# Performance work log

Hardware: AMD Instinct MI355X
Metric: run time of the kernel (lower is better)

## Reference

```python
import jax, jax.numpy as jnp
import numpy as np

B, T, S, H, V, MAXL = 8, 128, 256, 1024, 32000, 512
STD = 0.02


def _ln(x, g, b):
    m = jnp.mean(x, -1, keepdims=True)
    v = jnp.mean((x - m) ** 2, -1, keepdims=True)
    return (x - m) / jnp.sqrt(v + 1e-5) * g + b


def setup_inputs() -> dict:
    key = jax.random.key(0)
    ks = jax.random.split(key, 16)
    n = lambda k, shape: jax.random.normal(k, shape, jnp.float32) * STD
    inp = {
        "input_ids": jax.random.randint(ks[0], (B, T), 0, V),
        "encoder_hidden_states": jax.random.normal(ks[1], (B, S, H), jnp.float32),
        "pattern_masks": jax.random.randint(ks[2], (B, T, V), 0, 2).astype(bool),
        "attention_mask": jnp.ones((B, S), bool),
        "tok_emb": n(ks[3], (V, H)),
        "pos_emb": n(ks[4], (MAXL, H)),
        "w_ih": n(ks[5], (4 * H, H)),
        "w_hh": n(ks[6], (4 * H, H)),
        "b_ih": jnp.zeros((4 * H,), jnp.float32),
        "b_hh": jnp.zeros((4 * H,), jnp.float32),
        "wq": n(ks[7], (H, H)), "bq": jnp.zeros((H,), jnp.float32),
        "wk": n(ks[8], (H, H)), "bk": jnp.zeros((H,), jnp.float32),
        "wc": n(ks[9], (H, 2 * H)), "bc": jnp.zeros((H,), jnp.float32),
        "wo": n(ks[10], (V, H)), "bo": jnp.zeros((V,), jnp.float32),
        "g1": n(ks[11], (H,)), "be1": jnp.zeros((H,), jnp.float32),
        "g2": n(ks[12], (H,)), "be2": jnp.zeros((H,), jnp.float32),
    }
    return inp


def reference(input_ids, encoder_hidden_states, pattern_masks, attention_mask,
              tok_emb, pos_emb, w_ih, w_hh, b_ih, b_hh,
              wq, bq, wk, bk, wc, bc, wo, bo, g1, be1, g2, be2):
    # Token + positional embedding (dropout is identity in eval)
    x = tok_emb[input_ids] + pos_emb[:T][None, :, :]  # [B,T,H]

    # Single-layer LSTM (PyTorch gate order i,f,g,o) via scan over time
    def step(carry, xt):
        h, c = carry
        gates = xt @ w_ih.T + b_ih + h @ w_hh.T + b_hh
        i, f, g, o = jnp.split(gates, 4, axis=-1)
        c = jax.nn.sigmoid(f) * c + jax.nn.sigmoid(i) * jnp.tanh(g)
        h = jax.nn.sigmoid(o) * jnp.tanh(c)
        return (h, c), h

    h0 = jnp.zeros((B, H), x.dtype)
    _, hs = jax.lax.scan(step, (h0, h0), jnp.swapaxes(x, 0, 1))
    lstm_out = jnp.swapaxes(hs, 0, 1)  # [B,T,H]

    # Attention: per-position loop in torch == batched over T (keys invariant)
    qn = _ln(lstm_out @ wq.T + bq, g1, be1)              # [B,T,H]
    kn = _ln(encoder_hidden_states @ wk.T + bk, g1, be1)  # [B,S,H]
    scale = H ** (-0.5) * 0.5
    scores = jnp.einsum('bth,bsh->bts', qn, kn) * scale
    am = attention_mask[:, None, :]
    scores = jnp.where(am, scores, -10000.0)
    mx = jnp.max(scores, -1, keepdims=True)
    ex = jnp.exp(scores - mx)
    ex = jnp.where(am, ex, 0.0)
    w = ex / (jnp.sum(ex, -1, keepdims=True) + 1e-6)
    ctx = jnp.einsum('bts,bsh->bth', w, kn)              # [B,T,H]

    hidden = _ln(jnp.concatenate([lstm_out, ctx], -1) @ wc.T + bc, g2, be2)
    logits = hidden @ wo.T + bo                           # [B,T,V]
    logits = jnp.where(pattern_masks, logits, -10000.0)
    return logits
```

## Files before the change

### kernel.cpp

```cpp
#include <hip/hip_runtime.h>
#include <cstdint>
#include <cstddef>

#define Bdim 8
#define Tdim 128
#define Sdim 256
#define Hdim 1024
#define Vdim 32000
#define SENT 0xFFFFFFFFFFFFFFFFULL

typedef unsigned short u16;
typedef unsigned long long u64;
typedef __attribute__((ext_vector_type(8))) short short8;
typedef __attribute__((ext_vector_type(4))) short short4v;
typedef __attribute__((ext_vector_type(4))) float f32x4;
typedef __attribute__((ext_vector_type(2))) unsigned long long u64x2;

union Frag { short8 v; short4v h[2]; };

__device__ __forceinline__ float bf2f(u16 u){
  union { unsigned int i; float f; } x; x.i = ((unsigned int)u) << 16; return x.f;
}
__device__ __forceinline__ u16 f2b(float f){
  union { float f; unsigned int u; } x; x.f = f;
  unsigned int r = x.u + 0x7FFFu + ((x.u >> 16) & 1u);
  return (u16)(r >> 16);
}
__device__ __forceinline__ float ftanh(float x){
  x = fminf(10.f, fmaxf(-10.f, x));
  const float e = __expf(2.f * x);
  return (e - 1.f) / (e + 1.f);
}

__device__ __forceinline__ void gload16(const void* g, void* l){
  __builtin_amdgcn_global_load_lds((const __attribute__((address_space(1))) unsigned int*)g,
                                   (__attribute__((address_space(3))) unsigned int*)l, 16, 0, 0);
}

__device__ __forceinline__ int qsw(int r){ return (r + (r >> 2)) & 3; }

__device__ __forceinline__ u64 aload(const u64* p){
  return __hip_atomic_load(p, __ATOMIC_RELAXED, __HIP_MEMORY_SCOPE_AGENT);
}
__device__ __forceinline__ void astore(u64* p, u64 v){
  __hip_atomic_store(p, v, __ATOMIC_RELAXED, __HIP_MEMORY_SCOPE_AGENT);
}

__device__ __forceinline__ bool mask_at(const void* m, size_t idx, int byteflag){
  if (byteflag) return ((const unsigned char*)m)[idx] != 0;
  return ((const int*)m)[idx] != 0;
}

template<typename OutT, bool BF32, int MASK, int NT>
__device__ __forceinline__ void gemm_core(
    char* ldsA0, char* ldsB0, char* ldsA1, char* ldsB1,
    int m0, int n0, int z,
    const u16* __restrict__ A, int lda, long sA,
    const void* __restrict__ Bp, int ldb, long sB,
    OutT* __restrict__ C, int ldc, long sC,
    const float* __restrict__ bias,
    const void* __restrict__ mask,
    const int* __restrict__ mflag,
    int K, float alpha)
{
  const int tid  = threadIdx.x;
  const int lane = tid & 63, wid = tid >> 6;
  const int lm = lane & 15, lg = lane >> 4;
  const int wm = wid >> 1, wn = wid & 1;
  const char* Ab = (const char*)(A + (size_t)z * sA);

  f32x4 acc[4][4 * NT];
#pragma unroll
  for (int i = 0; i < 4; i++)
#pragma unroll
    for (int j = 0; j < 4 * NT; j++) acc[i][j] = (f32x4){0.f, 0.f, 0.f, 0.f};

  const int brow = tid >> 1, bhalf = tid & 1;
  const int qb_st = qsw(brow);

  auto stageA = [&](char* dst, int k0){
    const char* ga = Ab + ((size_t)m0 * lda + k0) * 2;
    const int f0 = tid, f1 = tid + 256;
    const int r0 = f0 >> 2, r1 = f1 >> 2;
    gload16(ga + (size_t)r0 * (lda * 2) + ((f0 & 3) ^ qsw(r0)) * 16, dst + (f0 & ~63) * 16);
    gload16(ga + (size_t)r1 * (lda * 2) + ((f1 & 3) ^ qsw(r1)) * 16, dst + (f1 & ~63) * 16);
  };
  auto stageB16 = [&](char* dst, int k0){
    const char* gbase = (const char*)((const u16*)Bp + (size_t)z * sB);
#pragma unroll
    for (int s = 0; s < NT; s++) {
      const char* gb = gbase + ((size_t)(n0 + s * 128) * ldb + k0) * 2;
      const int f0 = tid, f1 = tid + 256;
      const int r0 = f0 >> 2, r1 = f1 >> 2;
      gload16(gb + (size_t)r0 * (ldb * 2) + ((f0 & 3) ^ qsw(r0)) * 16, dst + s * 8192 + (f0 & ~63) * 16);
      gload16(gb + (size_t)r1 * (ldb * 2) + ((f1 & 3) ^ qsw(r1)) * 16, dst + s * 8192 + (f1 & ~63) * 16);
    }
  };

  float4 nv0, nv1, nv2, nv3;
  auto loadB32 = [&](int k0){
    const float* Bf = (const float*)Bp + (size_t)z * sB;
    const float4* src = (const float4*)(Bf + (size_t)(n0 + brow) * ldb + k0 + bhalf * 16);
    nv0 = src[0]; nv1 = src[1]; nv2 = src[2]; nv3 = src[3];
  };
  auto writeB32 = [&](char* dst){
    union { short8 v; short s[8]; } p0, p1;
    p0.s[0]=(short)f2b(nv0.x); p0.s[1]=(short)f2b(nv0.y); p0.s[2]=(short)f2b(nv0.z); p0.s[3]=(short)f2b(nv0.w);
    p0.s[4]=(short)f2b(nv1.x); p0.s[5]=(short)f2b(nv1.y); p0.s[6]=(short)f2b(nv1.z); p0.s[7]=(short)f2b(nv1.w);
    p1.s[0]=(short)f2b(nv2.x); p1.s[1]=(short)f2b(nv2.y); p1.s[2]=(short)f2b(nv2.z); p1.s[3]=(short)f2b(nv2.w);
    p1.s[4]=(short)f2b(nv3.x); p1.s[5]=(short)f2b(nv3.y); p1.s[6]=(short)f2b(nv3.z); p1.s[7]=(short)f2b(nv3.w);
    char* base = dst + brow * 64;
    *(short8*)(base + (((bhalf * 2 + 0) ^ qb_st) * 16)) = p0.v;
    *(short8*)(base + (((bhalf * 2 + 1) ^ qb_st) * 16)) = p1.v;
  };

  stageA(ldsA0, 0);
  if (BF32) { loadB32(0); writeB32(ldsB0); }
  else stageB16(ldsB0, 0);
  __syncthreads();

  char *cA = ldsA0, *cB = ldsB0, *nA = ldsA1, *nB = ldsB1;
  const int nk = K >> 5;
  for (int i = 0; i < nk; i++) {
    const bool more = (i + 1) < nk;
    if (more) {
      stageA(nA, (i + 1) << 5);
      if (BF32) loadB32((i + 1) << 5);
      else stageB16(nB, (i + 1) << 5);
    }
    Frag a[4];
#pragma unroll
    for (int mi = 0; mi < 4; mi++) {
      const int rr = wm * 64 + mi * 16 + lm;
      const int q = qsw(rr);
      const char* p = cA + rr * 64 + (lg & 1) * 8;
      a[mi].h[0] = *(const short4v*)(p + (((lg >> 1) ^ q) * 16));
      a[mi].h[1] = *(const short4v*)(p + ((((lg >> 1) | 2) ^ q) * 16));
    }
#pragma unroll
    for (int ni = 0; ni < 4 * NT; ni++) {
      const int s = ni >> 2, nl = ni & 3;
      const int rr = wn * 64 + nl * 16 + lm;
      const int q = qsw(rr);
      const char* p = cB + s * 8192 + rr * 64 + (lg & 1) * 8;
      Frag b;
      b.h[0] = *(const short4v*)(p + (((lg >> 1) ^ q) * 16));
      b.h[1] = *(const short4v*)(p + ((((lg >> 1) | 2) ^ q) * 16));
#pragma unroll
      for (int mi = 0; mi < 4; mi++)
        acc[mi][ni] = __builtin_amdgcn_mfma_f32_16x16x32_bf16(a[mi].v, b.v, acc[mi][ni], 0, 0, 0);
    }
    if (BF32 && more) writeB32(nB);
    __syncthreads();
    char* t;
    t = cA; cA = nA; nA = t;
    t = cB; cB = nB; nB = t;
  }

  const int bflag = (MASK == 1) ? *mflag : 0;
#pragma unroll
  for (int mi = 0; mi < 4; mi++) {
#pragma unroll
    for (int ni = 0; ni < 4 * NT; ni++) {
      const int row = m0 + wm * 64 + mi * 16 + lg * 4;
      const int col = n0 + (ni >> 2) * 128 + wn * 64 + (ni & 3) * 16 + lm;
      const float bb = bias ? bias[col] : 0.f;
#pragma unroll
      for (int j = 0; j < 4; j++) {
        float v = acc[mi][ni][j] * alpha + bb;
        const size_t midx = (size_t)(row + j) * ldc + col;
        if (MASK == 1) { if (!mask_at(mask, midx, bflag)) v = -10000.0f; }
        if (MASK == 2) { if (!((const unsigned char*)mask)[midx]) v = -10000.0f; }
        const size_t o = (size_t)z * sC + midx;
        if constexpr (sizeof(OutT) == 2) C[o] = (OutT)f2b(v); else C[o] = (OutT)v;
      }
    }
  }
}

template<typename OutT, bool BF32, int MASK, bool SWAP, int NT = 1>
__global__ __launch_bounds__(256) void gemm_bt(
    const u16* __restrict__ A, int lda, long sA,
    const void* __restrict__ Bp, int ldb, long sB,
    OutT* __restrict__ C, int ldc, long sC,
    const float* __restrict__ bias,
    const void* __restrict__ mask,
    const int* __restrict__ mflag,
    int K, float alpha)
{
  __shared__ alignas(16) char lds[(8192 + 8192 * NT) * 2];
  const int m0 = (SWAP ? blockIdx.x : blockIdx.y) * 128;
  const int n0 = (SWAP ? blockIdx.y : blockIdx.x) * (128 * NT);
  char* ldsA1 = lds + 8192 + 8192 * NT;
  gemm_core<OutT, BF32, MASK, NT>(lds, lds + 8192, ldsA1, ldsA1 + 8192,
      m0, n0, blockIdx.z, A, lda, sA, Bp, ldb, sB, C, ldc, sC,
      bias, mask, mflag, K, alpha);
}

__device__ void lstm_body(char* smem,
    const u16* __restrict__ xpre, const u16* __restrict__ whh,
    u16* __restrict__ hbuf, u16* __restrict__ cat, int bx)
{
  u16* wlds = (u16*)smem;
  u16* hlds = (u16*)(smem + 131072);
  const int tid = threadIdx.x, lane = tid & 63, wid = tid >> 6;
  const int lm = lane & 15, lg = lane >> 4;
  const int gcol0 = bx * 64;

  for (int q = tid; q < 8192; q += 256) {
    const int r = q >> 7, cc = q & 127;
    gload16(whh + (size_t)(gcol0 + r) * 1024 + (size_t)(cc ^ (r & 7)) * 8,
            (char*)wlds + (q & ~63) * 16);
  }

  float c_reg = 0.f;
  const int rloc = wid * 16 + lm, swb = rloc & 7, swa = lm & 7;
  const u16* wl = wlds + rloc * 1024;
  const u16* hl = hlds + swa * 1024;
  const int pk = tid >> 2, qq = tid & 3;
  const u16* xp = xpre + (size_t)(lm * Tdim) * 4096 + gcol0 + wid * 16 + lg * 4;

  for (int t = 0; t < Tdim; t++) {
    u64 xw = 0;
    if (lm < 8) xw = *(const u64*)(xp + (size_t)t * 4096);
    if (t > 0) {
      const u64* ps = (const u64*)(hbuf + ((size_t)(t - 1) * 64 + pk) * 128) + qq * 8;
      u64 w0=SENT,w1=SENT,w2=SENT,w3=SENT,w4=SENT,w5=SENT,w6=SENT,w7=SENT;
      for (;;) {
        if (w0 == SENT) w0 = aload(ps + 0);
        if (w1 == SENT) w1 = aload(ps + 1);
        if (w2 == SENT) w2 = aload(ps + 2);
        if (w3 == SENT) w3 = aload(ps + 3);
        if (w4 == SENT) w4 = aload(ps + 4);
        if (w5 == SENT) w5 = aload(ps + 5);
        if (w6 == SENT) w6 = aload(ps + 6);
        if (w7 == SENT) w7 = aload(ps + 7);
        if (w0 != SENT && w1 != SENT && w2 != SENT && w3 != SENT &&
            w4 != SENT && w5 != SENT && w6 != SENT && w7 != SENT) break;
        __builtin_amdgcn_s_sleep(1);
      }
      {
        const int m = qq * 2;
        u64x2 a; a[0] = w0; a[1] = w1;
        u64x2 b; b[0] = w2; b[1] = w3;
        *(u64x2*)((char*)hlds + m * 2048 + (((pk * 2 + 0) ^ m) * 16)) = a;
        *(u64x2*)((char*)hlds + m * 2048 + (((pk * 2 + 1) ^ m) * 16)) = b;
      }
      {
        const int m = qq * 2 + 1;
        u64x2 a; a[0] = w4; a[1] = w5;
        u64x2 b; b[0] = w6; b[1] = w7;
        *(u64x2*)((char*)hlds + m * 2048 + (((pk * 2 + 0) ^ m) * 16)) = a;
        *(u64x2*)((char*)hlds + m * 2048 + (((pk * 2 + 1) ^ m) * 16)) = b;
      }
    }
    __syncthreads();

    f32x4 acc0, acc1, acc2, acc3;
    {
      union { u64 w; u16 s[4]; } xu; xu.w = xw;
      acc0[0] = bf2f(xu.s[0]); acc0[1] = bf2f(xu.s[1]);
      acc0[2] = bf2f(xu.s[2]); acc0[3] = bf2f(xu.s[3]);
    }
    acc1 = (f32x4){0.f,0.f,0.f,0.f};
    acc2 = (f32x4){0.f,0.f,0.f,0.f};
    acc3 = (f32x4){0.f,0.f,0.f,0.f};

    if (t > 0) {
#pragma unroll
      for (int kk = 0; kk < 32; kk++) {
        const int c0 = kk * 4 + (lg >> 1);
        const int sub = (lg & 1) * 4;
        Frag aw, bh;
        aw.h[0] = *(const short4v*)(wl + ((c0 ^ swb) << 3) + sub);
        aw.h[1] = *(const short4v*)(wl + (((c0 + 2) ^ swb) << 3) + sub);
        bh.h[0] = *(const short4v*)(hl + ((c0 ^ swa) << 3) + sub);
        bh.h[1] = *(const short4v*)(hl + (((c0 + 2) ^ swa) << 3) + sub);
        if ((kk & 3) == 0)      acc0 = __builtin_amdgcn_mfma_f32_16x16x32_bf16(aw.v, bh.v, acc0, 0, 0, 0);
        else if ((kk & 3) == 1) acc1 = __builtin_amdgcn_mfma_f32_16x16x32_bf16(aw.v, bh.v, acc1, 0, 0, 0);
        else if ((kk & 3) == 2) acc2 = __builtin_amdgcn_mfma_f32_16x16x32_bf16(aw.v, bh.v, acc2, 0, 0, 0);
        else                    acc3 = __builtin_amdgcn_mfma_f32_16x16x32_bf16(aw.v, bh.v, acc3, 0, 0, 0);
      }
    }
    const f32x4 g4 = (acc0 + acc1) + (acc2 + acc3);

    const float si = 1.f / (1.f + __expf(-g4[0]));
    const float sf = 1.f / (1.f + __expf(-g4[1]));
    const float so = 1.f / (1.f + __expf(-g4[3]));
    const float cn = sf * c_reg + si * ftanh(g4[2]);
    c_reg = cn;
    const float hn = so * ftanh(cn);
    const int hb = (int)f2b(hn);

    const int v0 = __shfl(hb, lm, 64);
    const int v1 = __shfl(hb, lm + 16, 64);
    const int v2 = __shfl(hb, lm + 32, 64);
    const int v3 = __shfl(hb, lm + 48, 64);
    if (lg == 0 && lm < 8) {
      const u64 pack = (u64)(v0 & 0xFFFF) | ((u64)(v1 & 0xFFFF) << 16)
                     | ((u64)(v2 & 0xFFFF) << 32) | ((u64)(v3 & 0xFFFF) << 48);
      astore((u64*)(hbuf + ((size_t)t * 64 + bx) * 128 + lm * 16 + wid * 4), pack);
      *(u64*)(cat + (size_t)(lm * Tdim + t) * 2048 + bx * 16 + wid * 4) = pack;
    }
    __syncthreads();
  }
}

__global__ __launch_bounds__(256) void lstm_plus(
    const u16* __restrict__ xpre, const u16* __restrict__ whh,
    u16* __restrict__ hbuf, u16* __restrict__ cat,
    const u16* __restrict__ encb, const u16* __restrict__ wkb,
    float* __restrict__ klin, const float* __restrict__ bk,
    const float* __restrict__ wo, u16* __restrict__ wob,
    const float* __restrict__ wq, u16* __restrict__ wqb,
    const float* __restrict__ wc, u16* __restrict__ wcb,
    const void* __restrict__ pmask, unsigned char* __restrict__ pmaskb,
    const int* __restrict__ bflag)
{
  __shared__ alignas(16) char smem[147456];
  const int bx = blockIdx.x;
  if (bx < 64) {
    lstm_body(smem, xpre, whh, hbuf, cat, bx);
  } else if (bx < 192) {
    const int idx = bx - 64;
    gemm_core<float, false, 0, 1>(smem, smem + 8192, smem + 16384, smem + 24576,
        (idx >> 3) * 128, (idx & 7) * 128, 0,
        encb, 1024, 0, wkb, 1024, 0, klin, 1024, 0, bk, nullptr, nullptr, 1024, 1.f);
  } else {
    const int s = bx - 192;
    const int tid = threadIdx.x;
    for (int r = s; r < 1024; r += 64) {
      const size_t i = (size_t)r * 1024 + tid * 4;
      const float4 v = *(const float4*)(wq + i);
      u16* op = wqb + i;
      op[0] = f2b(v.x); op[1] = f2b(v.y); op[2] = f2b(v.z); op[3] = f2b(v.w);
    }
    for (int r = s; r < 1024; r += 64) {
#pragma unroll
      for (int hc = 0; hc < 2; hc++) {
        const size_t i = (size_t)r * 2048 + hc * 1024 + tid * 4;
        const float4 v = *(const float4*)(wc + i);
        u16* op = wcb + i;
        op[0] = f2b(v.x); op[1] = f2b(v.y); op[2] = f2b(v.z); op[3] = f2b(v.w);
      }
    }
    if (wob) {
      for (int r = s; r < Vdim; r += 64) {
        const size_t i = (size_t)r * 1024 + tid * 4;
        const float4 v = *(const float4*)(wo + i);
        u16* op = wob + i;
        op[0] = f2b(v.x); op[1] = f2b(v.y); op[2] = f2b(v.z); op[3] = f2b(v.w);
      }
    }
    if (pmaskb) {
      const int bfl = *bflag;
      const size_t total = (size_t)Bdim * Tdim * Vdim;
      const size_t nthr = 64 * 256;
      if (bfl == 0) {
        for (size_t i = ((size_t)s * 256 + tid) * 4; i < total; i += nthr * 4) {
          const int4 v = *(const int4*)((const int*)pmask + i);
          uchar4 o;
          o.x = v.x ? 1 : 0; o.y = v.y ? 1 : 0; o.z = v.z ? 1 : 0; o.w = v.w ? 1 : 0;
          *(uchar4*)(pmaskb + i) = o;
        }
      } else {
        for (size_t i = ((size_t)s * 256 + tid) * 16; i < total; i += nthr * 16) {
          *(int4*)(pmaskb + i) = *(const int4*)((const unsigned char*)pmask + i);
        }
      }
    }
  }
}

__global__ __launch_bounds__(256) void prep_k(
    const float* __restrict__ w_hh, const float* __restrict__ w_ih,
    const float* __restrict__ wk,   const float* __restrict__ enc,
    const int* __restrict__ ids,
    const float* __restrict__ tok,  const float* __restrict__ pos,
    const float* __restrict__ b_ih, const float* __restrict__ b_hh,
    const unsigned char* __restrict__ pmask,
    u16* __restrict__ whhb, u16* __restrict__ wihb, u16* __restrict__ wkb,
    u16* __restrict__ encb, u16* __restrict__ xbf,
    float* __restrict__ biasf, u64* __restrict__ hbuf, int* __restrict__ bflag)
{
  __shared__ int sdet;
  const int b = blockIdx.x, tid = threadIdx.x;
  if (b < 8192) {
    const bool ih = b >= 4096;
    const int r = b & 4095;
    const int p = (r & 3) * Hdim + (r >> 2);
    const float4 v = *(const float4*)((ih ? w_ih : w_hh) + (size_t)p * Hdim + tid * 4);
    u16* op = (ih ? wihb : whhb) + (size_t)r * Hdim + tid * 4;
    op[0] = f2b(v.x); op[1] = f2b(v.y); op[2] = f2b(v.z); op[3] = f2b(v.w);
  } else if (b < 9216) {
    const size_t i = (size_t)(b - 8192) * 1024 + tid * 4;
    const float4 v = *(const float4*)(wk + i);
    u16* op = wkb + i;
    op[0] = f2b(v.x); op[1] = f2b(v.y); op[2] = f2b(v.z); op[3] = f2b(v.w);
  } else if (b < 11264) {
    const size_t i = (size_t)(b - 9216) * 1024 + tid * 4;
    const float4 v = *(const float4*)(enc + i);
    u16* op = encb + i;
    op[0] = f2b(v.x); op[1] = f2b(v.y); op[2] = f2b(v.z); op[3] = f2b(v.w);
  } else if (b < 12288) {
    const int row = b - 11264;
    const int t = row & (Tdim - 1);
    const int id = ids[row];
    const int h0 = tid * 4;
    const float4 a = *(const float4*)(tok + (size_t)id * Hdim + h0);
    const float4 p = *(const float4*)(pos + (size_t)t * Hdim + h0);
    u16* op = xbf + (size_t)row * Hdim + h0;
    op[0] = f2b(a.x + p.x); op[1] = f2b(a.y + p.y); op[2] = f2b(a.z + p.z); op[3] = f2b(a.w + p.w);
  } else if (b < 12292) {
    const int n0 = (b - 12288) * 1024 + tid * 4;
#pragma unroll
    for (int j = 0; j < 4; j++) {
      const int n = n0 + j;
      const int p = (n & 3) * Hdim + (n >> 2);
      biasf[n] = b_ih[p] + b_hh[p];
    }
  } else if (b < 12548) {
    const size_t i = ((size_t)(b - 12292) * 256 + tid) * 4;
    u64x2 s2; s2[0] = SENT; s2[1] = SENT;
    *(u64x2*)(hbuf + i)     = s2;
    *(u64x2*)(hbuf + i + 2) = s2;
  } else {
    if (tid == 0) sdet = 0;
    __syncthreads();
    int loc = 0;
    for (int i = tid; i < 65536; i += 256)
      if ((i & 3) && pmask[i]) loc = 1;
    if (loc) atomicOr(&sdet, 1);
    __syncthreads();
    if (tid == 0) bflag[0] = sdet;
  }
}

__global__ __launch_bounds__(256) void ln_rows(const float* __restrict__ in, u16* __restrict__ out,
                                               const float* __restrict__ g, const float* __restrict__ be){
  const int row = blockIdx.x, tid = threadIdx.x;
  const int lane = tid & 63, wid = tid >> 6;
  const float4 x = *(const float4*)(in + (size_t)row * Hdim + tid * 4);
  float s = x.x + x.y + x.z + x.w;
  float q = x.x * x.x + x.y * x.y + x.z * x.z + x.w * x.w;
  for (int o = 32; o; o >>= 1) { s += __shfl_down(s, o, 64); q += __shfl_down(q, o, 64); }
  __shared__ float sm[8];
  if (lane == 0) { sm[wid] = s; sm[4 + wid] = q; }
  __syncthreads();
  const float ts = sm[0] + sm[1] + sm[2] + sm[3];
  const float tq = sm[4] + sm[5] + sm[6] + sm[7];
  const float mean = ts * (1.f / Hdim);
  const float var  = tq * (1.f / Hdim) - mean * mean;
  const float r = rsqrtf(var + 1e-5f);
  const int h0 = tid * 4;
  const float4 gv = *(const float4*)(g + h0);
  const float4 bv = *(const float4*)(be + h0);
  u16* op = out + (size_t)row * Hdim + h0;
  op[0] = f2b((x.x - mean) * r * gv.x + bv.x);
  op[1] = f2b((x.y - mean) * r * gv.y + bv.y);
  op[2] = f2b((x.z - mean) * r * gv.z + bv.z);
  op[3] = f2b((x.w - mean) * r * gv.w + bv.w);
}
__global__ __launch_bounds__(256) void softmax_k(const float* __restrict__ sc, const void* __restrict__ am,
                                                 const int* __restrict__ mflag, u16* __restrict__ w){
  const int row = blockIdx.x, tid = threadIdx.x;
  const int lane = tid & 63, wid = tid >> 6;
  const int b = row >> 7;
  const int bflag = *mflag;
  const float v = sc[(size_t)row * Sdim + tid];
  const bool mk = mask_at(am, (size_t)b * Sdim + tid, bflag);
  const float vm = mk ? v : -10000.0f;
  float mx = vm;
  for (int o = 32; o; o >>= 1) mx = fmaxf(mx, __shfl_down(mx, o, 64));
  __shared__ float sm[8];
  if (lane == 0) sm[wid] = mx;
  __syncthreads();
  mx = fmaxf(fmaxf(sm[0], sm[1]), fmaxf(sm[2], sm[3]));
  const float ex = mk ? expf(vm - mx) : 0.f;
  float ss = ex;
  for (int o = 32; o; o >>= 1) ss += __shfl_down(ss, o, 64);
  if (lane == 0) sm[4 + wid] = ss;
  __syncthreads();
  const float tot = sm[4] + sm[5] + sm[6] + sm[7];
  w[(size_t)row * Sdim + tid] = f2b(ex / (tot + 1e-6f));
}
__global__ __launch_bounds__(256) void transp_k(const u16* __restrict__ kn, u16* __restrict__ knT){
  __shared__ u16 tile[64][65];
  const int b = blockIdx.z, h0 = blockIdx.x * 64, s0 = blockIdx.y * 64;
  const u16* src = kn  + (size_t)b * Sdim * Hdim;
  u16* dst       = knT + (size_t)b * Hdim * Sdim;
  for (int e = threadIdx.x; e < 4096; e += 256) {
    const int r = e >> 6, c = e & 63;
    tile[r][c] = src[(size_t)(s0 + r) * Hdim + h0 + c];
  }
  __syncthreads();
  for (int e = threadIdx.x; e < 4096; e += 256) {
    const int hr = e >> 6, scc = e & 63;
    dst[(size_t)(h0 + hr) * Sdim + s0 + scc] = tile[scc][hr];
  }
}

extern "C" void kernel_launch(void* const* d_in, const int* in_sizes, int n_in,
                              void* d_out, int out_size, void* d_ws, size_t ws_size,
                              hipStream_t stream) {
  const int*   input_ids = (const int*)d_in[0];
  const float* enc   = (const float*)d_in[1];
  const void*  pmask = d_in[2];
  const void*  amask = d_in[3];
  const float* tok  = (const float*)d_in[4];
  const float* pos  = (const float*)d_in[5];
  const float* w_ih = (const float*)d_in[6];
  const float* w_hh = (const float*)d_in[7];
  const float* b_ih = (const float*)d_in[8];
  const float* b_hh = (const float*)d_in[9];
  const float* wq = (const float*)d_in[10];
  const float* bq = (const float*)d_in[11];
  const float* wk = (const float*)d_in[12];
  const float* bk = (const float*)d_in[13];
  const float* wc = (const float*)d_in[14];
  const float* bc = (const float*)d_in[15];
  const float* wo = (const float*)d_in[16];
  const float* bo = (const float*)d_in[17];
  const float* g1  = (const float*)d_in[18];
  const float* be1 = (const float*)d_in[19];
  const float* g2  = (const float*)d_in[20];
  const float* be2 = (const float*)d_in[21];
  float* out = (float*)d_out;

  char* ws = (char*)d_ws;
  size_t off = 0;
  auto alloc = [&](size_t b){ size_t o = off; off += (b + 255) & ~(size_t)255; return o; };
  u16*   whhb  = (u16*)  (ws + alloc((size_t)4096 * 1024 * 2));
  u16*   wihb  = (u16*)  (ws + alloc((size_t)4096 * 1024 * 2));
  u16*   wqb   = (u16*)  (ws + alloc((size_t)1024 * 1024 * 2));
  u16*   wkb   = (u16*)  (ws + alloc((size_t)1024 * 1024 * 2));
  u16*   wcb   = (u16*)  (ws + alloc((size_t)1024 * 2048 * 2));
  float* biasf = (float*)(ws + alloc(4096 * 4));
  u16*   xbf   = (u16*)  (ws + alloc((size_t)1024 * 1024 * 2));
  u16*   encb  = (u16*)  (ws + alloc((size_t)2048 * 1024 * 2));
  u16*   xpre  = (u16*)  (ws + alloc((size_t)1024 * 4096 * 2));
  u16*   hbuf  = (u16*)  (ws + alloc((size_t)Tdim * 64 * 128 * 2));
  u16*   cat   = (u16*)  (ws + alloc((size_t)1024 * 2048 * 2));
  float* qlin  = (float*)(ws + alloc((size_t)1024 * 1024 * 4));
  u16*   qn    = (u16*)  (ws + alloc((size_t)1024 * 1024 * 2));
  float* klin  = (float*)(ws + alloc((size_t)2048 * 1024 * 4));
  u16*   kn    = (u16*)  (ws + alloc((size_t)2048 * 1024 * 2));
  u16*   knT   = (u16*)  (ws + alloc((size_t)2048 * 1024 * 2));
  float* scores= (float*)(ws + alloc((size_t)8 * 128 * 256 * 4));
  u16*   attw  = (u16*)  (ws + alloc((size_t)8 * 128 * 256 * 2));
  float* hlin  = (float*)(ws + alloc((size_t)1024 * 1024 * 4));
  u16*   hid   = (u16*)  (ws + alloc((size_t)1024 * 1024 * 2));
  int*   bflag = (int*)  (ws + alloc(256));
  unsigned char* pmaskb = (unsigned char*)(ws + alloc((size_t)Bdim * Tdim * Vdim));
  const bool havePak = off <= ws_size;
  u16*   wob   = (u16*)  (ws + alloc((size_t)Vdim * Hdim * 2));
  const bool haveWob = off <= ws_size;
  if (!havePak) pmaskb = nullptr;
  if (!haveWob) wob = nullptr;
  (void)in_sizes; (void)n_in; (void)out_size;

  prep_k<<<12549, 256, 0, stream>>>(w_hh, w_ih, wk, enc, input_ids,
      tok, pos, b_ih, b_hh, (const unsigned char*)pmask,
      whhb, wihb, wkb, encb, xbf, biasf, (u64*)hbuf, bflag);

  gemm_bt<u16, false, 0, false><<<dim3(32, 8, 1), 256, 0, stream>>>(
      xbf, 1024, 0, wihb, 1024, 0, xpre, 4096, 0, biasf, nullptr, nullptr, 1024, 1.f);

  lstm_plus<<<256, 256, 0, stream>>>(xpre, whhb, hbuf, cat, encb, wkb, klin, bk,
                                     wo, wob, wq, wqb, wc, wcb, pmask, pmaskb, bflag);

  gemm_bt<float, false, 0, false><<<dim3(8, 8, 1), 256, 0, stream>>>(
      cat, 2048, 0, wqb, 1024, 0, qlin, 1024, 0, bq, nullptr, nullptr, 1024, 1.f);
  ln_rows<<<1024, 256, 0, stream>>>(qlin, qn, g1, be1);
  ln_rows<<<2048, 256, 0, stream>>>(klin, kn, g1, be1);
  transp_k<<<dim3(16, 4, 8), 256, 0, stream>>>(kn, knT);

  gemm_bt<float, false, 0, false><<<dim3(2, 1, 8), 256, 0, stream>>>(
      qn, 1024, 131072, kn, 1024, 262144, scores, 256, 32768, nullptr, nullptr, nullptr, 1024, 0.015625f);
  softmax_k<<<1024, 256, 0, stream>>>(scores, amask, bflag, attw);
  gemm_bt<u16, false, 0, false><<<dim3(8, 1, 8), 256, 0, stream>>>(
      attw, 256, 32768, knT, 256, 262144, cat + 1024, 2048, 262144, nullptr, nullptr, nullptr, 256, 1.f);

  gemm_bt<float, false, 0, false><<<dim3(8, 8, 1), 256, 0, stream>>>(
      cat, 2048, 0, wcb, 2048, 0, hlin, 1024, 0, bc, nullptr, nullptr, 2048, 1.f);
  ln_rows<<<1024, 256, 0, stream>>>(hlin, hid, g2, be2);

  if (wob && pmaskb)
    gemm_bt<float, false, 2, true><<<dim3(8, 250, 1), 256, 0, stream>>>(
        hid, 1024, 0, wob, 1024, 0, out, 32000, 0, bo, pmaskb, nullptr, 1024, 1.f);
  else if (wob)
    gemm_bt<float, false, 1, true><<<dim3(8, 250, 1), 256, 0, stream>>>(
        hid, 1024, 0, wob, 1024, 0, out, 32000, 0, bo, pmask, bflag, 1024, 1.f);
  else
    gemm_bt<float, true, 1, true><<<dim3(8, 250, 1), 256, 0, stream>>>(
        hid, 1024, 0, wo, 1024, 0, out, 32000, 0, bo, pmask, bflag, 1024, 1.f);
}
```

Before: 800.6 us.

## Use 256x256 tile GEMM for masked vocab projection and fuse Q/K layernorms

Adds a dedicated 512-thread GEMM kernel with 256x256 output tiles for the final vocab projection, so each loaded A/B tile is reused across more MFMAs and fewer blocks re-read the operands. It removes the unused NT template parameter from the generic GEMM. The two layernorm launches for queries and keys are merged into one launch. The larger tile uses 64KB of LDS and more accumulator registers, which may reduce occupancy, and the grid shrinks to 500 blocks.

```diff
diff --git a/kernel.cpp b/kernel.cpp
--- a/kernel.cpp
+++ b/kernel.cpp
@@ -51,7 +51,7 @@
   return ((const int*)m)[idx] != 0;
 }
 
-template<typename OutT, bool BF32, int MASK, int NT>
+template<typename OutT, bool BF32, int MASK>
 __device__ __forceinline__ void gemm_core(
     char* ldsA0, char* ldsB0, char* ldsA1, char* ldsB1,
     int m0, int n0, int z,
@@ -69,11 +69,11 @@
   const int wm = wid >> 1, wn = wid & 1;
   const char* Ab = (const char*)(A + (size_t)z * sA);
 
-  f32x4 acc[4][4 * NT];
+  f32x4 acc[4][4];
 #pragma unroll
   for (int i = 0; i < 4; i++)
 #pragma unroll
-    for (int j = 0; j < 4 * NT; j++) acc[i][j] = (f32x4){0.f, 0.f, 0.f, 0.f};
+    for (int j = 0; j < 4; j++) acc[i][j] = (f32x4){0.f, 0.f, 0.f, 0.f};
 
   const int brow = tid >> 1, bhalf = tid & 1;
   const int qb_st = qsw(brow);
@@ -86,15 +86,11 @@
     gload16(ga + (size_t)r1 * (lda * 2) + ((f1 & 3) ^ qsw(r1)) * 16, dst + (f1 & ~63) * 16);
   };
   auto stageB16 = [&](char* dst, int k0){
-    const char* gbase = (const char*)((const u16*)Bp + (size_t)z * sB);
-#pragma unroll
-    for (int s = 0; s < NT; s++) {
-      const char* gb = gbase + ((size_t)(n0 + s * 128) * ldb + k0) * 2;
-      const int f0 = tid, f1 = tid + 256;
-      const int r0 = f0 >> 2, r1 = f1 >> 2;
-      gload16(gb + (size_t)r0 * (ldb * 2) + ((f0 & 3) ^ qsw(r0)) * 16, dst + s * 8192 + (f0 & ~63) * 16);
-      gload16(gb + (size_t)r1 * (ldb * 2) + ((f1 & 3) ^ qsw(r1)) * 16, dst + s * 8192 + (f1 & ~63) * 16);
-    }
+    const char* gb = (const char*)((const u16*)Bp + (size_t)z * sB) + ((size_t)n0 * ldb + k0) * 2;
+    const int f0 = tid, f1 = tid + 256;
+    const int r0 = f0 >> 2, r1 = f1 >> 2;
+    gload16(gb + (size_t)r0 * (ldb * 2) + ((f0 & 3) ^ qsw(r0)) * 16, dst + (f0 & ~63) * 16);
+    gload16(gb + (size_t)r1 * (ldb * 2) + ((f1 & 3) ^ qsw(r1)) * 16, dst + (f1 & ~63) * 16);
   };
 
   float4 nv0, nv1, nv2, nv3;
@@ -138,11 +134,10 @@
       a[mi].h[1] = *(const short4v*)(p + ((((lg >> 1) | 2) ^ q) * 16));
     }
 #pragma unroll
-    for (int ni = 0; ni < 4 * NT; ni++) {
-      const int s = ni >> 2, nl = ni & 3;
-      const int rr = wn * 64 + nl * 16 + lm;
+    for (int ni = 0; ni < 4; ni++) {
+      const int rr = wn * 64 + ni * 16 + lm;
       const int q = qsw(rr);
-      const char* p = cB + s * 8192 + rr * 64 + (lg & 1) * 8;
+      const char* p = cB + rr * 64 + (lg & 1) * 8;
       Frag b;
       b.h[0] = *(const short4v*)(p + (((lg >> 1) ^ q) * 16));
       b.h[1] = *(const short4v*)(p + ((((lg >> 1) | 2) ^ q) * 16));
@@ -161,9 +156,9 @@
 #pragma unroll
   for (int mi = 0; mi < 4; mi++) {
 #pragma unroll
-    for (int ni = 0; ni < 4 * NT; ni++) {
+    for (int ni = 0; ni < 4; ni++) {
       const int row = m0 + wm * 64 + mi * 16 + lg * 4;
-      const int col = n0 + (ni >> 2) * 128 + wn * 64 + (ni & 3) * 16 + lm;
+      const int col = n0 + wn * 64 + ni * 16 + lm;
       const float bb = bias ? bias[col] : 0.f;
 #pragma unroll
       for (int j = 0; j < 4; j++) {
@@ -178,7 +173,7 @@
   }
 }
 
-template<typename OutT, bool BF32, int MASK, bool SWAP, int NT = 1>
+template<typename OutT, bool BF32, int MASK, bool SWAP>
 __global__ __launch_bounds__(256) void gemm_bt(
     const u16* __restrict__ A, int lda, long sA,
     const void* __restrict__ Bp, int ldb, long sB,
@@ -188,13 +183,104 @@
     const int* __restrict__ mflag,
     int K, float alpha)
 {
-  __shared__ alignas(16) char lds[(8192 + 8192 * NT) * 2];
+  __shared__ alignas(16) char lds[32768];
   const int m0 = (SWAP ? blockIdx.x : blockIdx.y) * 128;
-  const int n0 = (SWAP ? blockIdx.y : blockIdx.x) * (128 * NT);
-  char* ldsA1 = lds + 8192 + 8192 * NT;
-  gemm_core<OutT, BF32, MASK, NT>(lds, lds + 8192, ldsA1, ldsA1 + 8192,
+  const int n0 = (SWAP ? blockIdx.y : blockIdx.x) * 128;
+  gemm_core<OutT, BF32, MASK>(lds, lds + 8192, lds + 16384, lds + 24576,
       m0, n0, blockIdx.z, A, lda, sA, Bp, ldb, sB, C, ldc, sC,
       bias, mask, mflag, K, alpha);
+}
+
+__global__ __launch_bounds__(512) void gemm256_mask(
+    const u16* __restrict__ A, int lda,
+    const u16* __restrict__ Bt, int ldb,
+    float* __restrict__ C, int ldc,
+    const float* __restrict__ bias,
+    const unsigned char* __restrict__ mask,
+    int K)
+{
+  __shared__ alignas(16) char lds[65536];
+  char* ldsA0 = lds;
+  char* ldsB0 = lds + 16384;
+  char* ldsA1 = lds + 32768;
+  char* ldsB1 = lds + 49152;
+  const int tid  = threadIdx.x;
+  const int lane = tid & 63, wid = tid >> 6;
+  const int lm = lane & 15, lg = lane >> 4;
+  const int wm = wid >> 2, wn = wid & 3;
+  const int m0 = blockIdx.x * 256, n0 = blockIdx.y * 256;
+  const char* Ab = (const char*)A + (size_t)m0 * lda * 2;
+  const char* Bb = (const char*)Bt + (size_t)n0 * ldb * 2;
+
+  f32x4 acc[8][4];
+#pragma unroll
+  for (int i = 0; i < 8; i++)
+#pragma unroll
+    for (int j = 0; j < 4; j++) acc[i][j] = (f32x4){0.f, 0.f, 0.f, 0.f};
+
+  auto stageT = [&](const char* G, int ld, char* dst, int k0){
+    const char* g = G + (size_t)k0 * 2;
+    const int f0 = tid, f1 = tid + 512;
+    const int r0 = f0 >> 2, r1 = f1 >> 2;
+    gload16(g + (size_t)r0 * (ld * 2) + ((f0 & 3) ^ qsw(r0)) * 16, dst + (f0 & ~63) * 16);
+    gload16(g + (size_t)r1 * (ld * 2) + ((f1 & 3) ^ qsw(r1)) * 16, dst + (f1 & ~63) * 16);
+  };
+
+  stageT(Ab, lda, ldsA0, 0);
+  stageT(Bb, ldb, ldsB0, 0);
+  __syncthreads();
+
+  char *cA = ldsA0, *cB = ldsB0, *nA = ldsA1, *nB = ldsB1;
+  const int nk = K >> 5;
+  for (int i = 0; i < nk; i++) {
+    const bool more = (i + 1) < nk;
+    if (more) {
+      stageT(Ab, lda, nA, (i + 1) << 5);
+      stageT(Bb, ldb, nB, (i + 1) << 5);
+    }
+    Frag a[8];
+#pragma unroll
+    for (int mi = 0; mi < 8; mi++) {
+      const int rr = wm * 128 + mi * 16 + lm;
+      const int q = qsw(rr);
+      const char* p = cA + rr * 64 + (lg & 1) * 8;
+      a[mi].h[0] = *(const short4v*)(p + (((lg >> 1) ^ q) * 16));
+      a[mi].h[1] = *(const short4v*)(p + ((((lg >> 1) | 2) ^ q) * 16));
+    }
+#pragma unroll
+    for (int ni = 0; ni < 4; ni++) {
+      const int rr = wn * 64 + ni * 16 + lm;
+      const int q = qsw(rr);
+      const char* p = cB + rr * 64 + (lg & 1) * 8;
+      Frag b;
+      b.h[0] = *(const short4v*)(p + (((lg >> 1) ^ q) * 16));
+      b.h[1] = *(const short4v*)(p + ((((lg >> 1) | 2) ^ q) * 16));
+#pragma unroll
+      for (int mi = 0; mi < 8; mi++)
+        acc[mi][ni] = __builtin_amdgcn_mfma_f32_16x16x32_bf16(a[mi].v, b.v, acc[mi][ni], 0, 0, 0);
+    }
+    __syncthreads();
+    char* t;
+    t = cA; cA = nA; nA = t;
+    t = cB; cB = nB; nB = t;
+  }
+
+#pragma unroll
+  for (int mi = 0; mi < 8; mi++) {
+#pragma unroll
+    for (int ni = 0; ni < 4; ni++) {
+      const int row = m0 + wm * 128 + mi * 16 + lg * 4;
+      const int col = n0 + wn * 64 + ni * 16 + lm;
+      const float bb = bias[col];
+#pragma unroll
+      for (int j = 0; j < 4; j++) {
+        float v = acc[mi][ni][j] + bb;
+        const size_t midx = (size_t)(row + j) * ldc + col;
+        if (!mask[midx]) v = -10000.0f;
+        C[midx] = v;
+      }
+    }
+  }
 }
 
 __device__ void lstm_body(char* smem,
@@ -323,7 +409,7 @@
     lstm_body(smem, xpre, whh, hbuf, cat, bx);
   } else if (bx < 192) {
     const int idx = bx - 64;
-    gemm_core<float, false, 0, 1>(smem, smem + 8192, smem + 16384, smem + 24576,
+    gemm_core<float, false, 0>(smem, smem + 8192, smem + 16384, smem + 24576,
         (idx >> 3) * 128, (idx & 7) * 128, 0,
         encb, 1024, 0, wkb, 1024, 0, klin, 1024, 0, bk, nullptr, nullptr, 1024, 1.f);
   } else {
@@ -436,9 +522,10 @@
   }
 }
 
-__global__ __launch_bounds__(256) void ln_rows(const float* __restrict__ in, u16* __restrict__ out,
-                                               const float* __restrict__ g, const float* __restrict__ be){
-  const int row = blockIdx.x, tid = threadIdx.x;
+__device__ __forceinline__ void ln_row_body(const float* __restrict__ in, u16* __restrict__ out,
+                                            int row, const float* __restrict__ g,
+                                            const float* __restrict__ be){
+  const int tid = threadIdx.x;
   const int lane = tid & 63, wid = tid >> 6;
   const float4 x = *(const float4*)(in + (size_t)row * Hdim + tid * 4);
   float s = x.x + x.y + x.z + x.w;
@@ -460,6 +547,17 @@
   op[1] = f2b((x.y - mean) * r * gv.y + bv.y);
   op[2] = f2b((x.z - mean) * r * gv.z + bv.z);
   op[3] = f2b((x.w - mean) * r * gv.w + bv.w);
+}
+__global__ __launch_bounds__(256) void ln_rows(const float* __restrict__ in, u16* __restrict__ out,
+                                               const float* __restrict__ g, const float* __restrict__ be){
+  ln_row_body(in, out, blockIdx.x, g, be);
+}
+__global__ __launch_bounds__(256) void ln_qk(const float* __restrict__ qlin, u16* __restrict__ qn,
+                                             const float* __restrict__ klin, u16* __restrict__ kn,
+                                             const float* __restrict__ g, const float* __restrict__ be){
+  const int row = blockIdx.x;
+  if (row < 1024) ln_row_body(qlin, qn, row, g, be);
+  else            ln_row_body(klin, kn, row - 1024, g, be);
 }
 __global__ __launch_bounds__(256) void softmax_k(const float* __restrict__ sc, const void* __restrict__ am,
                                                  const int* __restrict__ mflag, u16* __restrict__ w){
@@ -571,8 +669,7 @@
 
   gemm_bt<float, false, 0, false><<<dim3(8, 8, 1), 256, 0, stream>>>(
       cat, 2048, 0, wqb, 1024, 0, qlin, 1024, 0, bq, nullptr, nullptr, 1024, 1.f);
-  ln_rows<<<1024, 256, 0, stream>>>(qlin, qn, g1, be1);
-  ln_rows<<<2048, 256, 0, stream>>>(klin, kn, g1, be1);
+  ln_qk<<<3072, 256, 0, stream>>>(qlin, qn, klin, kn, g1, be1);
   transp_k<<<dim3(16, 4, 8), 256, 0, stream>>>(kn, knT);
 
   gemm_bt<float, false, 0, false><<<dim3(2, 1, 8), 256, 0, stream>>>(
@@ -586,8 +683,8 @@
   ln_rows<<<1024, 256, 0, stream>>>(hlin, hid, g2, be2);
 
   if (wob && pmaskb)
-    gemm_bt<float, false, 2, true><<<dim3(8, 250, 1), 256, 0, stream>>>(
-        hid, 1024, 0, wob, 1024, 0, out, 32000, 0, bo, pmaskb, nullptr, 1024, 1.f);
+    gemm256_mask<<<dim3(4, 125, 1), 512, 0, stream>>>(
+        hid, 1024, wob, 1024, out, 32000, bo, pmaskb, 1024);
   else if (wob)
     gemm_bt<float, false, 1, true><<<dim3(8, 250, 1), 256, 0, stream>>>(
         hid, 1024, 0, wob, 1024, 0, out, 32000, 0, bo, pmask, bflag, 1024, 1.f);
```

After: 793.7 us. Within noise of the previous version (-0.9%).
